# Optimization experiments

Measured on AMD Instinct MI355X. Metric: run time of the kernel, lower is better.

The kernel has to match this reference:

```python
import jax, jax.numpy as jnp
import numpy as np

B, S, V, E, H, L = 32, 512, 32000, 256, 512, 48


def setup_inputs() -> dict:
    key = jax.random.key(0)
    ks = jax.random.split(key, 12)
    tokens = jax.random.randint(ks[0], (B, S), 0, V)
    length = jax.random.randint(ks[1], (B,), S // 2, S + 1)
    labels = jax.random.randint(ks[2], (B, S), 0, L)
    embed_table = jax.random.normal(ks[3], (V, E), jnp.float32) * 0.1
    embed_table = embed_table.at[0].set(0.0)  # padding_idx = 0
    # torch LSTM gate order: i, f, g, o ; b = b_ih + b_hh folded together
    w_ih_f = jax.random.normal(ks[4], (4 * H, E), jnp.float32) * 0.05
    w_hh_f = jax.random.normal(ks[5], (4 * H, H), jnp.float32) * 0.05
    b_f = jnp.zeros((4 * H,), jnp.float32)
    w_ih_b = jax.random.normal(ks[6], (4 * H, E), jnp.float32) * 0.05
    w_hh_b = jax.random.normal(ks[7], (4 * H, H), jnp.float32) * 0.05
    b_b = jnp.zeros((4 * H,), jnp.float32)
    w_em = jax.random.normal(ks[8], (L, 2 * H), jnp.float32) * 0.02
    b_em = jnp.zeros((L,), jnp.float32)
    transition = jax.random.uniform(ks[9], (L, L), jnp.float32)  # torch.rand init
    return {"tokens": tokens, "length": length, "labels": labels,
            "embed_table": embed_table,
            "w_ih_f": w_ih_f, "w_hh_f": w_hh_f, "b_f": b_f,
            "w_ih_b": w_ih_b, "w_hh_b": w_hh_b, "b_b": b_b,
            "w_em": w_em, "b_em": b_em, "transition": transition}


def _lstm_dir(x, w_ih, w_hh, b, reverse):
    # x: [B,S,E] -> hidden states [B,S,H]
    xw = jnp.einsum('bse,ge->bsg', x, w_ih) + b  # precompute input projection [B,S,4H]
    if reverse:
        xw = xw[:, ::-1]
    Bn = x.shape[0]
    Hn = w_hh.shape[1]
    h0 = jnp.zeros((Bn, Hn), x.dtype)
    c0 = jnp.zeros((Bn, Hn), x.dtype)

    def step(carry, xt):
        h, c = carry
        gates = xt + h @ w_hh.T  # [B,4H]
        i, f, g, o = jnp.split(gates, 4, axis=-1)
        i = jax.nn.sigmoid(i)
        f = jax.nn.sigmoid(f)
        g = jnp.tanh(g)
        o = jax.nn.sigmoid(o)
        c = f * c + i * g
        h = o * jnp.tanh(c)
        return (h, c), h

    _, hs = jax.lax.scan(step, (h0, c0), jnp.swapaxes(xw, 0, 1))
    hs = jnp.swapaxes(hs, 0, 1)  # [B,S,H]
    if reverse:
        hs = hs[:, ::-1]
    return hs


def reference(tokens, length, labels, embed_table,
              w_ih_f, w_hh_f, b_f, w_ih_b, w_hh_b, b_b,
              w_em, b_em, transition):
    x = embed_table[tokens]                      # [B,S,E]
    hf = _lstm_dir(x, w_ih_f, w_hh_f, b_f, reverse=False)
    hb = _lstm_dir(x, w_ih_b, w_hh_b, b_b, reverse=True)
    h = jnp.concatenate([hf, hb], axis=-1)       # [B,S,2H]
    logits = jnp.einsum('bsh,lh->bsl', h, w_em) + b_em
    e = jnp.exp(logits)                          # emission = exp(linear), as in source
    T = jnp.exp(transition)                      # transition = exp(param), as in source
    Bn, Sn = tokens.shape
    pos = jnp.arange(Sn)[None, :]
    mask = pos < length[:, None]                 # [B,S] valid positions

    # gold path score: sum emissions over valid steps + transitions between them
    em_real = jnp.take_along_axis(e, labels[..., None], axis=-1)[..., 0]  # [B,S]
    real = jnp.sum(em_real * mask, axis=-1)
    trans_real = T[labels[:, :-1], labels[:, 1:]]                          # [B,S-1]
    real = real + jnp.sum(trans_real * mask[:, 1:], axis=-1)

    # forward algorithm, exactly as written in source:
    # alpha_new[k] = logsumexp_l( alpha[k] + T[k,l] + e_t[l] )
    alpha0 = e[:, 0, :]                          # [B,L]

    def step(alpha, inp):
        et, mt = inp                             # [B,L], [B]
        scores = alpha[:, :, None] + T[None, :, :] + et[:, None, :]  # [B,L,L]
        new = jax.nn.logsumexp(scores, axis=-1)
        alpha = jnp.where(mt[:, None], new, alpha)
        return alpha, None

    alpha, _ = jax.lax.scan(step, alpha0,
                            (jnp.swapaxes(e[:, 1:], 0, 1),
                             jnp.swapaxes(mask[:, 1:], 0, 1)))
    sum_score = jax.nn.logsumexp(alpha, axis=-1)  # [B]
    return sum_score - real                       # negative log probability per example
```

## Files before the change

kernel.cpp:

```cpp
#include <hip/hip_runtime.h>
#include <math.h>
#include <stdint.h>

#define Bn 32
#define Sn 512
#define En 256
#define Hn 512
#define Ln 48
#define G4 2048
#define NWG 32
#define SENT16 0x7FFFu

typedef unsigned short u16;
typedef __attribute__((ext_vector_type(8))) __bf16 bf16x8;
typedef __attribute__((ext_vector_type(4))) float f32x4;

__device__ inline float bf2f(u16 u) {
    return __uint_as_float(((unsigned)u) << 16);
}
__device__ inline u16 f2bf(float f) {
    unsigned u = __float_as_uint(f);
    unsigned r = (u + 0x7fffu + ((u >> 16) & 1u)) >> 16;
    return (u16)r;
}
__device__ inline float sigmoidf_(float x) { return 1.f / (1.f + expf(-x)); }
__device__ inline float tanh_fast(float x) { return 2.f / (1.f + expf(-2.f * x)) - 1.f; }

__device__ inline unsigned badMask(f32x4 v) {
    unsigned acc = 0;
    #pragma unroll
    for (int i = 0; i < 4; i++) {
        unsigned d = __float_as_uint(v[i]);
        unsigned x = d ^ 0x7FFF7FFFu;
        acc |= (x - 0x00010001u) & ~x & 0x80008000u;
    }
    return acc;
}

__global__ __launch_bounds__(256) void prep_kernel(
    const int* __restrict__ tokens, const float* __restrict__ embed,
    const float* __restrict__ wihf, const float* __restrict__ wihb,
    const float* __restrict__ whhf, const float* __restrict__ whhb,
    const float* __restrict__ wem, const float* __restrict__ trans,
    u16* __restrict__ xbf, u16* __restrict__ wihf_b, u16* __restrict__ wihb_b,
    u16* __restrict__ whhf_b, u16* __restrict__ whhb_b, u16* __restrict__ wem_b,
    float* __restrict__ expT, float* __restrict__ alphaAcc,
    float* __restrict__ realAcc, unsigned* __restrict__ hf32,
    unsigned* __restrict__ hb32)
{
    size_t idx = (size_t)blockIdx.x * blockDim.x + threadIdx.x;
    size_t stride = (size_t)gridDim.x * blockDim.x;
    for (size_t i = idx; i < (size_t)Bn * Sn * En; i += stride) {
        size_t n = i >> 8; int ee = (int)(i & 255);
        int tok = tokens[n];
        xbf[i] = f2bf(embed[(size_t)tok * En + ee]);
    }
    for (size_t i = idx; i < (size_t)G4 * En; i += stride) {
        wihf_b[i] = f2bf(wihf[i]); wihb_b[i] = f2bf(wihb[i]);
    }
    for (size_t i = idx; i < (size_t)G4 * Hn; i += stride) {
        whhf_b[i] = f2bf(whhf[i]); whhb_b[i] = f2bf(whhb[i]);
    }
    for (size_t i = idx; i < (size_t)Ln * 2 * Hn; i += stride) wem_b[i] = f2bf(wem[i]);
    for (size_t i = idx; i < (size_t)Ln * Ln; i += stride) expT[i] = expf(trans[i]);
    for (size_t i = idx; i < (size_t)Bn * Ln; i += stride) alphaAcc[i] = 0.f;
    for (size_t i = idx; i < (size_t)Bn; i += stride) realAcc[i] = 0.f;
    const unsigned sp = (SENT16 << 16) | SENT16;
    for (size_t i = idx; i < (size_t)Bn * Sn * Hn / 2; i += stride) {
        hf32[i] = sp; hb32[i] = sp;
    }
}

__global__ __launch_bounds__(256) void gemm_xw(
    const u16* __restrict__ xbf, const u16* __restrict__ wihf_b,
    const u16* __restrict__ wihb_b, const float* __restrict__ bias_f,
    const float* __restrict__ bias_b, u16* __restrict__ xw_f, u16* __restrict__ xw_b)
{
    int mb = blockIdx.x, nb = blockIdx.y, dir = blockIdx.z;
    const u16* wih = dir ? wihb_b : wihf_b;
    const float* bias = dir ? bias_b : bias_f;
    u16* xw = dir ? xw_b : xw_f;

    __shared__ u16 As[128 * 72];
    __shared__ u16 Bs[128 * 72];

    int tid = threadIdx.x;
    int w = tid >> 6, lane = tid & 63;
    int lm = lane & 15, kq = lane >> 4;
    int Moff = (w & 1) * 64, Noff = (w >> 1) * 64;

    f32x4 zero = {0.f, 0.f, 0.f, 0.f};
    f32x4 acc[4][4];
    #pragma unroll
    for (int mi = 0; mi < 4; mi++)
        #pragma unroll
        for (int ni = 0; ni < 4; ni++) acc[mi][ni] = zero;

    for (int kc = 0; kc < 4; kc++) {
        #pragma unroll
        for (int it = 0; it < 4; it++) {
            int idx = tid + it * 256;
            int r = idx >> 3, pos = (idx & 7) * 8;
            *(bf16x8*)&As[r * 72 + pos] =
                *(const bf16x8*)&xbf[((size_t)(mb * 128 + r)) * En + kc * 64 + pos];
            *(bf16x8*)&Bs[r * 72 + pos] =
                *(const bf16x8*)&wih[((size_t)(nb * 128 + r)) * En + kc * 64 + pos];
        }
        __syncthreads();
        #pragma unroll
        for (int ks = 0; ks < 2; ks++) {
            int k = ks * 32 + kq * 8;
            bf16x8 af[4], bfr[4];
            #pragma unroll
            for (int mi = 0; mi < 4; mi++)
                af[mi] = *(const bf16x8*)&As[(Moff + mi * 16 + lm) * 72 + k];
            #pragma unroll
            for (int ni = 0; ni < 4; ni++)
                bfr[ni] = *(const bf16x8*)&Bs[(Noff + ni * 16 + lm) * 72 + k];
            #pragma unroll
            for (int mi = 0; mi < 4; mi++)
                #pragma unroll
                for (int ni = 0; ni < 4; ni++)
                    acc[mi][ni] = __builtin_amdgcn_mfma_f32_16x16x32_bf16(
                        af[mi], bfr[ni], acc[mi][ni], 0, 0, 0);
        }
        __syncthreads();
    }
    #pragma unroll
    for (int mi = 0; mi < 4; mi++)
        #pragma unroll
        for (int ni = 0; ni < 4; ni++)
            #pragma unroll
            for (int reg = 0; reg < 4; reg++) {
                int row = Moff + mi * 16 + kq * 4 + reg;
                int col = Noff + ni * 16 + lm;
                int n = mb * 128 + row;
                int g = nb * 128 + col;
                int t = n & 511, b = n >> 9;
                float v = acc[mi][ni][reg] + bias[g];
                xw[((size_t)t * Bn + b) * G4 + g] = f2bf(v);
            }
}

__global__ __launch_bounds__(512) void lstm_rec(
    const u16* __restrict__ whhf_b, const u16* __restrict__ whhb_b,
    const u16* __restrict__ xw_f, const u16* __restrict__ xw_b,
    u16* __restrict__ hf, u16* __restrict__ hb)
{
    int wg = blockIdx.x;
    int dir = wg >> 5;
    int w = wg & 31;
    const u16* __restrict__ whh = dir ? whhb_b : whhf_b;
    const u16* __restrict__ xw  = dir ? xw_b  : xw_f;
    u16* __restrict__ hbuf = dir ? hb : hf;

    __shared__ u16 Hs[32 * 512];
    __shared__ float Cp[4 * 32 * 17];
    __shared__ u16 hout[32 * 16];

    int tid = threadIdx.x;
    int wv = tid >> 6, lane = tid & 63;
    int lm = lane & 15, kq = lane >> 4;
    int mt = wv & 1, nt = wv >> 1;
    int b = tid >> 4, hc = tid & 15;

    bf16x8 Bf[16];
    {
        const u16* wrow = &whh[((size_t)nt * Hn + (size_t)w * 16 + lm) * Hn];
        #pragma unroll
        for (int ks = 0; ks < 16; ks++)
            Bf[ks] = *(const bf16x8*)&wrow[ks * 32 + kq * 8];
    }

    float c_state = 0.f;
    const f32x4 zero = {0.f, 0.f, 0.f, 0.f};

    for (int it = 0; it < Sn; it++) {
        int t = dir ? (Sn - 1 - it) : it;
        f32x4 acc = zero;

        const u16* xp = &xw[((size_t)t * Bn + b) * G4 + (size_t)w * 16 + hc];
        float xg0 = bf2f(xp[0 * Hn]);
        float xg1 = bf2f(xp[1 * Hn]);
        float xg2 = bf2f(xp[2 * Hn]);
        float xg3 = bf2f(xp[3 * Hn]);

        if (it > 0) {
            int tprev = dir ? (t + 1) : (t - 1);
            const u16* base = &hbuf[((size_t)b * Sn + tprev) * Hn];
            const u16* p0 = base + (hc + 0) * 8;
            const u16* p1 = base + (hc + 16) * 8;
            const u16* p2 = base + (hc + 32) * 8;
            const u16* p3 = base + (hc + 48) * 8;
            f32x4 h0, h1, h2, h3;
            int tries = 0;
            while (true) {
                asm volatile(
                    "global_load_dwordx4 %0, %4, off sc1\n\t"
                    "global_load_dwordx4 %1, %5, off sc1\n\t"
                    "global_load_dwordx4 %2, %6, off sc1\n\t"
                    "global_load_dwordx4 %3, %7, off sc1\n\t"
                    "s_waitcnt vmcnt(0)"
                    : "=v"(h0), "=v"(h1), "=v"(h2), "=v"(h3)
                    : "v"(p0), "v"(p1), "v"(p2), "v"(p3)
                    : "memory");
                if (!(badMask(h0) | badMask(h1) | badMask(h2) | badMask(h3))) break;
                if (++tries > (1 << 16)) break;
            }
            *(f32x4*)&Hs[(b * 64 + ((hc + 0) ^ (b & 7))) * 8] = h0;
            *(f32x4*)&Hs[(b * 64 + ((hc + 16) ^ (b & 7))) * 8] = h1;
            *(f32x4*)&Hs[(b * 64 + ((hc + 32) ^ (b & 7))) * 8] = h2;
            *(f32x4*)&Hs[(b * 64 + ((hc + 48) ^ (b & 7))) * 8] = h3;
            __syncthreads();

            f32x4 aa = zero, ab = zero;
            #pragma unroll
            for (int ks2 = 0; ks2 < 8; ks2++) {
                bf16x8 a0 = *(const bf16x8*)
                    &Hs[((mt * 16 + lm) * 64 + (((2 * ks2) * 4 + kq) ^ (lm & 7))) * 8];
                aa = __builtin_amdgcn_mfma_f32_16x16x32_bf16(a0, Bf[2 * ks2], aa, 0, 0, 0);
                bf16x8 a1 = *(const bf16x8*)
                    &Hs[((mt * 16 + lm) * 64 + (((2 * ks2 + 1) * 4 + kq) ^ (lm & 7))) * 8];
                ab = __builtin_amdgcn_mfma_f32_16x16x32_bf16(a1, Bf[2 * ks2 + 1], ab, 0, 0, 0);
            }
            acc = aa + ab;
        }

        #pragma unroll
        for (int reg = 0; reg < 4; reg++)
            Cp[(nt * 32 + mt * 16 + kq * 4 + reg) * 17 + lm] = acc[reg];
        __syncthreads();

        float g0 = Cp[(0 * 32 + b) * 17 + hc] + xg0;
        float g1 = Cp[(1 * 32 + b) * 17 + hc] + xg1;
        float g2 = Cp[(2 * 32 + b) * 17 + hc] + xg2;
        float g3 = Cp[(3 * 32 + b) * 17 + hc] + xg3;
        float i_ = sigmoidf_(g0);
        float f_ = sigmoidf_(g1);
        float gg = tanh_fast(g2);
        float o_ = sigmoidf_(g3);
        c_state = f_ * c_state + i_ * gg;
        float hv = o_ * tanh_fast(c_state);
        hout[tid] = f2bf(hv);
        __syncthreads();

        if (tid < 64) {
            int bq = lane >> 1, half = lane & 1;
            f32x4 hv8 = *(const f32x4*)&hout[lane * 8];
            u16* sp = &hbuf[((size_t)bq * Sn + t) * Hn + (size_t)w * 16 + half * 8];
            asm volatile("global_store_dwordx4 %0, %1, off sc1"
                         :: "v"(sp), "v"(hv8) : "memory");
        }
    }
}

__global__ __launch_bounds__(256) void emis_crf(
    const u16* __restrict__ hf, const u16* __restrict__ hb,
    const u16* __restrict__ wem_b, const float* __restrict__ bem,
    const float* __restrict__ expT, const int* __restrict__ labels,
    const int* __restrict__ lengths, float* __restrict__ e0,
    float* __restrict__ alphaAcc, float* __restrict__ realAcc)
{
    int mb = blockIdx.x;
    int b = mb >> 3, t0 = (mb & 7) * 64;

    __shared__ float eL[64][49];
    __shared__ float Ts[48 * 48];
    __shared__ float sred[4][48];
    __shared__ float rred[64];

    int tid = threadIdx.x;
    for (int i = tid; i < 48 * 48; i += 256) Ts[i] = expT[i];

    int wv = tid >> 6, lane = tid & 63;
    int lm = lane & 15, lkq = (lane >> 4) * 8;
    int row = mb * 64 + wv * 16;

    f32x4 zero = {0.f, 0.f, 0.f, 0.f};
    f32x4 acc[3] = {zero, zero, zero};
    for (int ks = 0; ks < 32; ks++) {
        int k = ks * 32 + lkq;
        const u16* hsrc = (ks < 16) ? &hf[(size_t)(row + lm) * Hn + k]
                                    : &hb[(size_t)(row + lm) * Hn + (k - 512)];
        bf16x8 a = *(const bf16x8*)hsrc;
        #pragma unroll
        for (int nt = 0; nt < 3; nt++) {
            bf16x8 bfr = *(const bf16x8*)&wem_b[(size_t)(nt * 16 + lm) * 1024 + k];
            acc[nt] = __builtin_amdgcn_mfma_f32_16x16x32_bf16(a, bfr, acc[nt], 0, 0, 0);
        }
    }
    #pragma unroll
    for (int nt = 0; nt < 3; nt++)
        #pragma unroll
        for (int reg = 0; reg < 4; reg++) {
            int rib = wv * 16 + (lane >> 4) * 4 + reg;
            int col = nt * 16 + lm;
            float v = expf(acc[nt][reg] + bem[col]);
            eL[rib][col] = v;
            if ((mb & 7) == 0 && rib == 0) e0[b * Ln + col] = v;
        }
    __syncthreads();

    int len = lengths[b];
    if (tid < 192) {
        int i = tid % 48, tg = tid / 48;
        float sacc = 0.f;
        for (int p = tg * 16; p < tg * 16 + 16; p++) {
            int t = t0 + p;
            if (t >= 1 && t < len) {
                float m = -1e30f;
                for (int j = 0; j < 48; j++) m = fmaxf(m, Ts[i * 48 + j] + eL[p][j]);
                float s = 0.f;
                for (int j = 0; j < 48; j++) s += expf(Ts[i * 48 + j] + eL[p][j] - m);
                sacc += m + logf(s);
            }
        }
        sred[tg][i] = sacc;
    } else {
        int p = tid - 192;
        int t = t0 + p;
        float r = 0.f;
        if (t < len) {
            int lab = labels[b * Sn + t];
            r = eL[p][lab];
            if (t >= 1) r += Ts[labels[b * Sn + t - 1] * 48 + lab];
        }
        rred[p] = r;
    }
    __syncthreads();
    if (tid < 48) {
        float s = sred[0][tid] + sred[1][tid] + sred[2][tid] + sred[3][tid];
        atomicAdd(&alphaAcc[b * Ln + tid], s);
    } else if (tid == 48) {
        float r = 0.f;
        for (int p = 0; p < 64; p++) r += rred[p];
        atomicAdd(&realAcc[b], r);
    }
}

__global__ __launch_bounds__(64) void finalize(
    const float* __restrict__ e0, const float* __restrict__ alphaAcc,
    const float* __restrict__ realAcc, float* __restrict__ out)
{
    int b = threadIdx.x;
    if (b >= Bn) return;
    float m = -1e30f;
    for (int i = 0; i < Ln; i++) {
        float a = e0[b * Ln + i] + alphaAcc[b * Ln + i];
        m = fmaxf(m, a);
    }
    float s = 0.f;
    for (int i = 0; i < Ln; i++) {
        float a = e0[b * Ln + i] + alphaAcc[b * Ln + i];
        s += expf(a - m);
    }
    out[b] = m + logf(s) - realAcc[b];
}

extern "C" void kernel_launch(void* const* d_in, const int* in_sizes, int n_in,
                              void* d_out, int out_size, void* d_ws, size_t ws_size,
                              hipStream_t stream)
{
    const int*   tokens = (const int*)d_in[0];
    const int*   length = (const int*)d_in[1];
    const int*   labels = (const int*)d_in[2];
    const float* embed  = (const float*)d_in[3];
    const float* wihf   = (const float*)d_in[4];
    const float* whhf   = (const float*)d_in[5];
    const float* bf     = (const float*)d_in[6];
    const float* wihb   = (const float*)d_in[7];
    const float* whhb   = (const float*)d_in[8];
    const float* bbv    = (const float*)d_in[9];
    const float* wem    = (const float*)d_in[10];
    const float* bem    = (const float*)d_in[11];
    const float* trans  = (const float*)d_in[12];
    float* out = (float*)d_out;

    char* p = (char*)d_ws;
    auto take = [&](size_t bytes) -> char* {
        char* q = p;
        p += (bytes + 255) & ~(size_t)255;
        return q;
    };
    u16* xw_f   = (u16*)take((size_t)Sn * Bn * G4 * 2);
    u16* xw_b   = (u16*)take((size_t)Sn * Bn * G4 * 2);
    u16* hf     = (u16*)take((size_t)Bn * Sn * Hn * 2);
    u16* hb     = (u16*)take((size_t)Bn * Sn * Hn * 2);
    u16* xbf    = (u16*)take((size_t)Bn * Sn * En * 2);
    u16* wihf_b = (u16*)take((size_t)G4 * En * 2);
    u16* wihb_b = (u16*)take((size_t)G4 * En * 2);
    u16* whhf_b = (u16*)take((size_t)G4 * Hn * 2);
    u16* whhb_b = (u16*)take((size_t)G4 * Hn * 2);
    u16* wem_b  = (u16*)take((size_t)Ln * 2 * Hn * 2);
    float* expT     = (float*)take((size_t)Ln * Ln * 4);
    float* e0       = (float*)take((size_t)Bn * Ln * 4);
    float* alphaAcc = (float*)take((size_t)Bn * Ln * 4);
    float* realAcc  = (float*)take((size_t)Bn * 4);
    if ((size_t)(p - (char*)d_ws) > ws_size) return;

    prep_kernel<<<4096, 256, 0, stream>>>(tokens, embed, wihf, wihb, whhf, whhb, wem, trans,
                                          xbf, wihf_b, wihb_b, whhf_b, whhb_b, wem_b,
                                          expT, alphaAcc, realAcc,
                                          (unsigned*)hf, (unsigned*)hb);

    dim3 g1(128, 16, 2);
    gemm_xw<<<g1, 256, 0, stream>>>(xbf, wihf_b, wihb_b, bf, bbv, xw_f, xw_b);

    void* ra[] = { (void*)&whhf_b, (void*)&whhb_b, (void*)&xw_f, (void*)&xw_b,
                   (void*)&hf, (void*)&hb };
    hipLaunchCooperativeKernel((const void*)lstm_rec, dim3(2 * NWG), dim3(512), ra, 0, stream);

    emis_crf<<<256, 256, 0, stream>>>(hf, hb, wem_b, bem, expT, labels, length,
                                      e0, alphaAcc, realAcc);
    finalize<<<1, 64, 0, stream>>>(e0, alphaAcc, realAcc, out);
}
```

Before: 1.810 ms.

## Interleave forward and backward LSTM directions in each workgroup with async LDS prefetch

Each of 32 workgroups now runs both the forward and the backward recurrence, alternating half-steps, instead of 64 workgroups each running one direction. While one direction computes, the hidden-state row the other direction needs is prefetched straight into LDS with global_load_lds. Afterwards it is checked for the sentinel and reloaded only if it is stale. The aim is to hide the cross-workgroup global-memory latency on the serial critical path. In exchange, each workgroup does twice the serial work, holds twice the weight registers, and gives up half the parallelism.

```diff
diff --git a/kernel.cpp b/kernel.cpp
--- a/kernel.cpp
+++ b/kernel.cpp
@@ -35,6 +35,57 @@
         acc |= (x - 0x00010001u) & ~x & 0x80008000u;
     }
     return acc;
+}
+
+__device__ inline void wg_barrier() {
+    asm volatile("s_waitcnt lgkmcnt(0)" ::: "memory");
+    __builtin_amdgcn_s_barrier();
+    asm volatile("" ::: "memory");
+}
+__device__ inline void wg_barrier_vm() {
+    asm volatile("s_waitcnt vmcnt(0) lgkmcnt(0)" ::: "memory");
+    __builtin_amdgcn_s_barrier();
+    asm volatile("" ::: "memory");
+}
+
+__device__ inline void gl_lds16(const u16* gsrc, u16* ldst) {
+    __builtin_amdgcn_global_load_lds(
+        (const __attribute__((address_space(1))) unsigned int*)gsrc,
+        (__attribute__((address_space(3))) unsigned int*)ldst,
+        16, 0, 17);
+}
+
+__device__ inline void check_fix(u16* Hsbuf, const u16* rowbase, int b, int hc) {
+    int sw = b & 7;
+    u16* s0 = &Hsbuf[(b * 64 + (hc + 0)) * 8];
+    u16* s1 = &Hsbuf[(b * 64 + (hc + 16)) * 8];
+    u16* s2 = &Hsbuf[(b * 64 + (hc + 32)) * 8];
+    u16* s3 = &Hsbuf[(b * 64 + (hc + 48)) * 8];
+    f32x4 h0 = *(const f32x4*)s0;
+    f32x4 h1 = *(const f32x4*)s1;
+    f32x4 h2 = *(const f32x4*)s2;
+    f32x4 h3 = *(const f32x4*)s3;
+    if (badMask(h0) | badMask(h1) | badMask(h2) | badMask(h3)) {
+        const u16* p0 = rowbase + (size_t)((hc + 0) ^ sw) * 8;
+        const u16* p1 = rowbase + (size_t)((hc + 16) ^ sw) * 8;
+        const u16* p2 = rowbase + (size_t)((hc + 32) ^ sw) * 8;
+        const u16* p3 = rowbase + (size_t)((hc + 48) ^ sw) * 8;
+        int tries = 0;
+        for (;;) {
+            asm volatile(
+                "global_load_dwordx4 %0, %4, off sc1\n\t"
+                "global_load_dwordx4 %1, %5, off sc1\n\t"
+                "global_load_dwordx4 %2, %6, off sc1\n\t"
+                "global_load_dwordx4 %3, %7, off sc1\n\t"
+                "s_waitcnt vmcnt(0)"
+                : "=&v"(h0), "=&v"(h1), "=&v"(h2), "=&v"(h3)
+                : "v"(p0), "v"(p1), "v"(p2), "v"(p3)
+                : "memory");
+            if (!(badMask(h0) | badMask(h1) | badMask(h2) | badMask(h3))) break;
+            if (++tries > (1 << 16)) break;
+        }
+        *(f32x4*)s0 = h0; *(f32x4*)s1 = h1; *(f32x4*)s2 = h2; *(f32x4*)s3 = h3;
+    }
 }
 
 __global__ __launch_bounds__(256) void prep_kernel(
@@ -147,14 +198,10 @@
     const u16* __restrict__ xw_f, const u16* __restrict__ xw_b,
     u16* __restrict__ hf, u16* __restrict__ hb)
 {
-    int wg = blockIdx.x;
-    int dir = wg >> 5;
-    int w = wg & 31;
-    const u16* __restrict__ whh = dir ? whhb_b : whhf_b;
-    const u16* __restrict__ xw  = dir ? xw_b  : xw_f;
-    u16* __restrict__ hbuf = dir ? hb : hf;
-
-    __shared__ u16 Hs[32 * 512];
+    int w = blockIdx.x;
+
+    __shared__ u16 HsF[32 * 512];
+    __shared__ u16 HsB[32 * 512];
     __shared__ float Cp[4 * 32 * 17];
     __shared__ u16 hout[32 * 16];
 
@@ -164,90 +211,125 @@
     int mt = wv & 1, nt = wv >> 1;
     int b = tid >> 4, hc = tid & 15;
 
-    bf16x8 Bf[16];
+    bf16x8 BfF[16], BfB[16];
     {
-        const u16* wrow = &whh[((size_t)nt * Hn + (size_t)w * 16 + lm) * Hn];
-        #pragma unroll
-        for (int ks = 0; ks < 16; ks++)
-            Bf[ks] = *(const bf16x8*)&wrow[ks * 32 + kq * 8];
-    }
-
-    float c_state = 0.f;
+        const u16* wrF = &whhf_b[((size_t)nt * Hn + (size_t)w * 16 + lm) * Hn];
+        const u16* wrB = &whhb_b[((size_t)nt * Hn + (size_t)w * 16 + lm) * Hn];
+        #pragma unroll
+        for (int ks = 0; ks < 16; ks++) {
+            BfF[ks] = *(const bf16x8*)&wrF[ks * 32 + kq * 8];
+            BfB[ks] = *(const bf16x8*)&wrB[ks * 32 + kq * 8];
+        }
+    }
+
+    float cF = 0.f, cB = 0.f;
     const f32x4 zero = {0.f, 0.f, 0.f, 0.f};
 
     for (int it = 0; it < Sn; it++) {
-        int t = dir ? (Sn - 1 - it) : it;
+        int tf = it, tb = Sn - 1 - it;
+
+        wg_barrier_vm();
+        if (it > 0)
+            check_fix(HsF, &hf[((size_t)b * Sn + (tf - 1)) * Hn], b, hc);
+        const u16* xpf = &xw_f[((size_t)tf * Bn + b) * G4 + (size_t)w * 16 + hc];
+        u16 xg0 = xpf[0 * Hn], xg1 = xpf[1 * Hn], xg2 = xpf[2 * Hn], xg3 = xpf[3 * Hn];
+        if (it > 0) {
+            #pragma unroll
+            for (int c = 0; c < 4; c++) {
+                int bb = wv * 4 + c;
+                const u16* rowb = &hb[((size_t)bb * Sn + (tb + 1)) * Hn];
+                gl_lds16(rowb + (size_t)(lane ^ (bb & 7)) * 8, &HsB[bb * 512]);
+            }
+        }
+        wg_barrier();
         f32x4 acc = zero;
-
-        const u16* xp = &xw[((size_t)t * Bn + b) * G4 + (size_t)w * 16 + hc];
-        float xg0 = bf2f(xp[0 * Hn]);
-        float xg1 = bf2f(xp[1 * Hn]);
-        float xg2 = bf2f(xp[2 * Hn]);
-        float xg3 = bf2f(xp[3 * Hn]);
-
         if (it > 0) {
-            int tprev = dir ? (t + 1) : (t - 1);
-            const u16* base = &hbuf[((size_t)b * Sn + tprev) * Hn];
-            const u16* p0 = base + (hc + 0) * 8;
-            const u16* p1 = base + (hc + 16) * 8;
-            const u16* p2 = base + (hc + 32) * 8;
-            const u16* p3 = base + (hc + 48) * 8;
-            f32x4 h0, h1, h2, h3;
-            int tries = 0;
-            while (true) {
-                asm volatile(
-                    "global_load_dwordx4 %0, %4, off sc1\n\t"
-                    "global_load_dwordx4 %1, %5, off sc1\n\t"
-                    "global_load_dwordx4 %2, %6, off sc1\n\t"
-                    "global_load_dwordx4 %3, %7, off sc1\n\t"
-                    "s_waitcnt vmcnt(0)"
-                    : "=v"(h0), "=v"(h1), "=v"(h2), "=v"(h3)
-                    : "v"(p0), "v"(p1), "v"(p2), "v"(p3)
-                    : "memory");
-                if (!(badMask(h0) | badMask(h1) | badMask(h2) | badMask(h3))) break;
-                if (++tries > (1 << 16)) break;
-            }
-            *(f32x4*)&Hs[(b * 64 + ((hc + 0) ^ (b & 7))) * 8] = h0;
-            *(f32x4*)&Hs[(b * 64 + ((hc + 16) ^ (b & 7))) * 8] = h1;
-            *(f32x4*)&Hs[(b * 64 + ((hc + 32) ^ (b & 7))) * 8] = h2;
-            *(f32x4*)&Hs[(b * 64 + ((hc + 48) ^ (b & 7))) * 8] = h3;
-            __syncthreads();
-
             f32x4 aa = zero, ab = zero;
             #pragma unroll
             for (int ks2 = 0; ks2 < 8; ks2++) {
                 bf16x8 a0 = *(const bf16x8*)
-                    &Hs[((mt * 16 + lm) * 64 + (((2 * ks2) * 4 + kq) ^ (lm & 7))) * 8];
-                aa = __builtin_amdgcn_mfma_f32_16x16x32_bf16(a0, Bf[2 * ks2], aa, 0, 0, 0);
+                    &HsF[((mt * 16 + lm) * 64 + (((2 * ks2) * 4 + kq) ^ (lm & 7))) * 8];
+                aa = __builtin_amdgcn_mfma_f32_16x16x32_bf16(a0, BfF[2 * ks2], aa, 0, 0, 0);
                 bf16x8 a1 = *(const bf16x8*)
-                    &Hs[((mt * 16 + lm) * 64 + (((2 * ks2 + 1) * 4 + kq) ^ (lm & 7))) * 8];
-                ab = __builtin_amdgcn_mfma_f32_16x16x32_bf16(a1, Bf[2 * ks2 + 1], ab, 0, 0, 0);
+                    &HsF[((mt * 16 + lm) * 64 + (((2 * ks2 + 1) * 4 + kq) ^ (lm & 7))) * 8];
+                ab = __builtin_amdgcn_mfma_f32_16x16x32_bf16(a1, BfF[2 * ks2 + 1], ab, 0, 0, 0);
             }
             acc = aa + ab;
         }
-
         #pragma unroll
         for (int reg = 0; reg < 4; reg++)
             Cp[(nt * 32 + mt * 16 + kq * 4 + reg) * 17 + lm] = acc[reg];
-        __syncthreads();
-
-        float g0 = Cp[(0 * 32 + b) * 17 + hc] + xg0;
-        float g1 = Cp[(1 * 32 + b) * 17 + hc] + xg1;
-        float g2 = Cp[(2 * 32 + b) * 17 + hc] + xg2;
-        float g3 = Cp[(3 * 32 + b) * 17 + hc] + xg3;
-        float i_ = sigmoidf_(g0);
-        float f_ = sigmoidf_(g1);
-        float gg = tanh_fast(g2);
-        float o_ = sigmoidf_(g3);
-        c_state = f_ * c_state + i_ * gg;
-        float hv = o_ * tanh_fast(c_state);
-        hout[tid] = f2bf(hv);
-        __syncthreads();
-
+        wg_barrier();
+        {
+            float g0 = Cp[(0 * 32 + b) * 17 + hc] + bf2f(xg0);
+            float g1 = Cp[(1 * 32 + b) * 17 + hc] + bf2f(xg1);
+            float g2 = Cp[(2 * 32 + b) * 17 + hc] + bf2f(xg2);
+            float g3 = Cp[(3 * 32 + b) * 17 + hc] + bf2f(xg3);
+            float i_ = sigmoidf_(g0);
+            float f_ = sigmoidf_(g1);
+            float gg = tanh_fast(g2);
+            float o_ = sigmoidf_(g3);
+            cF = f_ * cF + i_ * gg;
+            hout[tid] = f2bf(o_ * tanh_fast(cF));
+        }
+        wg_barrier();
         if (tid < 64) {
             int bq = lane >> 1, half = lane & 1;
             f32x4 hv8 = *(const f32x4*)&hout[lane * 8];
-            u16* sp = &hbuf[((size_t)bq * Sn + t) * Hn + (size_t)w * 16 + half * 8];
+            u16* sp = &hf[((size_t)bq * Sn + tf) * Hn + (size_t)w * 16 + half * 8];
+            asm volatile("global_store_dwordx4 %0, %1, off sc1"
+                         :: "v"(sp), "v"(hv8) : "memory");
+        }
+
+        wg_barrier_vm();
+        if (it > 0)
+            check_fix(HsB, &hb[((size_t)b * Sn + (tb + 1)) * Hn], b, hc);
+        const u16* xpb = &xw_b[((size_t)tb * Bn + b) * G4 + (size_t)w * 16 + hc];
+        u16 yg0 = xpb[0 * Hn], yg1 = xpb[1 * Hn], yg2 = xpb[2 * Hn], yg3 = xpb[3 * Hn];
+        if (it < Sn - 1) {
+            #pragma unroll
+            for (int c = 0; c < 4; c++) {
+                int bb = wv * 4 + c;
+                const u16* rowf = &hf[((size_t)bb * Sn + tf) * Hn];
+                gl_lds16(rowf + (size_t)(lane ^ (bb & 7)) * 8, &HsF[bb * 512]);
+            }
+        }
+        wg_barrier();
+        acc = zero;
+        if (it > 0) {
+            f32x4 aa = zero, ab = zero;
+            #pragma unroll
+            for (int ks2 = 0; ks2 < 8; ks2++) {
+                bf16x8 a0 = *(const bf16x8*)
+                    &HsB[((mt * 16 + lm) * 64 + (((2 * ks2) * 4 + kq) ^ (lm & 7))) * 8];
+                aa = __builtin_amdgcn_mfma_f32_16x16x32_bf16(a0, BfB[2 * ks2], aa, 0, 0, 0);
+                bf16x8 a1 = *(const bf16x8*)
+                    &HsB[((mt * 16 + lm) * 64 + (((2 * ks2 + 1) * 4 + kq) ^ (lm & 7))) * 8];
+                ab = __builtin_amdgcn_mfma_f32_16x16x32_bf16(a1, BfB[2 * ks2 + 1], ab, 0, 0, 0);
+            }
+            acc = aa + ab;
+        }
+        #pragma unroll
+        for (int reg = 0; reg < 4; reg++)
+            Cp[(nt * 32 + mt * 16 + kq * 4 + reg) * 17 + lm] = acc[reg];
+        wg_barrier();
+        {
+            float g0 = Cp[(0 * 32 + b) * 17 + hc] + bf2f(yg0);
+            float g1 = Cp[(1 * 32 + b) * 17 + hc] + bf2f(yg1);
+            float g2 = Cp[(2 * 32 + b) * 17 + hc] + bf2f(yg2);
+            float g3 = Cp[(3 * 32 + b) * 17 + hc] + bf2f(yg3);
+            float i_ = sigmoidf_(g0);
+            float f_ = sigmoidf_(g1);
+            float gg = tanh_fast(g2);
+            float o_ = sigmoidf_(g3);
+            cB = f_ * cB + i_ * gg;
+            hout[tid] = f2bf(o_ * tanh_fast(cB));
+        }
+        wg_barrier();
+        if (tid >= 64 && tid < 128) {
+            int bq = lane >> 1, half = lane & 1;
+            f32x4 hv8 = *(const f32x4*)&hout[lane * 8];
+            u16* sp = &hb[((size_t)bq * Sn + tb) * Hn + (size_t)w * 16 + half * 8];
             asm volatile("global_store_dwordx4 %0, %1, off sc1"
                          :: "v"(sp), "v"(hv8) : "memory");
         }
@@ -408,7 +490,7 @@
 
     void* ra[] = { (void*)&whhf_b, (void*)&whhb_b, (void*)&xw_f, (void*)&xw_b,
                    (void*)&hf, (void*)&hb };
-    hipLaunchCooperativeKernel((const void*)lstm_rec, dim3(2 * NWG), dim3(512), ra, 0, stream);
+    hipLaunchCooperativeKernel((const void*)lstm_rec, dim3(NWG), dim3(512), ra, 0, stream);
 
     emis_crf<<<256, 256, 0, stream>>>(hf, hb, wem_b, bem, expT, labels, length,
                                       e0, alphaAcc, realAcc);
```

Result: slower. 2.767 ms (+52.8%).

## Place each LSTM direction on a single XCD via claim-based team assignment

Applied to the files above, without the earlier changes.

Replaces the cooperative launch with an oversubscribed grid where workgroups read their XCC id, claim slots per XCD, and the first two XCDs to fill 32 slots become the forward and backward teams. Keeping a direction's 32 workgroups on one XCD lets hidden-state exchange go through that XCD's shared L2, so polling first uses sc0 loads and stores are written at both scopes. This removes cross-XCD coherence latency from the per-step recurrence sync. The cost is extra idle workgroups, spin-waits on role assignment, a risk of deadlock if an XCD cannot hold 32 resident workgroups, and dependence on the hardware dispatch pattern.

```diff
diff --git a/kernel.cpp b/kernel.cpp
--- a/kernel.cpp
+++ b/kernel.cpp
@@ -8,7 +8,7 @@
 #define Hn 512
 #define Ln 48
 #define G4 2048
-#define NWG 32
+#define CLAIM_G 1024
 #define SENT16 0x7FFFu
 
 typedef unsigned short u16;
@@ -46,7 +46,8 @@
     u16* __restrict__ whhf_b, u16* __restrict__ whhb_b, u16* __restrict__ wem_b,
     float* __restrict__ expT, float* __restrict__ alphaAcc,
     float* __restrict__ realAcc, unsigned* __restrict__ hf32,
-    unsigned* __restrict__ hb32)
+    unsigned* __restrict__ hb32, int* __restrict__ claimCnt,
+    int* __restrict__ teamCnt, int* __restrict__ teamRole)
 {
     size_t idx = (size_t)blockIdx.x * blockDim.x + threadIdx.x;
     size_t stride = (size_t)gridDim.x * blockDim.x;
@@ -65,6 +66,8 @@
     for (size_t i = idx; i < (size_t)Ln * Ln; i += stride) expT[i] = expf(trans[i]);
     for (size_t i = idx; i < (size_t)Bn * Ln; i += stride) alphaAcc[i] = 0.f;
     for (size_t i = idx; i < (size_t)Bn; i += stride) realAcc[i] = 0.f;
+    for (size_t i = idx; i < 16; i += stride) { claimCnt[i] = 0; teamRole[i] = 0; }
+    for (size_t i = idx; i < 1; i += stride) teamCnt[0] = 0;
     const unsigned sp = (SENT16 << 16) | SENT16;
     for (size_t i = idx; i < (size_t)Bn * Sn * Hn / 2; i += stride) {
         hf32[i] = sp; hb32[i] = sp;
@@ -145,11 +148,48 @@
 __global__ __launch_bounds__(512) void lstm_rec(
     const u16* __restrict__ whhf_b, const u16* __restrict__ whhb_b,
     const u16* __restrict__ xw_f, const u16* __restrict__ xw_b,
-    u16* __restrict__ hf, u16* __restrict__ hb)
-{
-    int wg = blockIdx.x;
-    int dir = wg >> 5;
-    int w = wg & 31;
+    u16* __restrict__ hf, u16* __restrict__ hb,
+    int* __restrict__ claimCnt, int* __restrict__ teamCnt,
+    int* __restrict__ teamRole)
+{
+    __shared__ int roleS[2];
+    int tid = threadIdx.x;
+
+    if (tid == 0) {
+        unsigned xcdr;
+        asm volatile("s_getreg_b32 %0, hwreg(HW_REG_XCC_ID)" : "=s"(xcdr));
+        int myx = (int)(xcdr & 15);
+        int slot = __hip_atomic_fetch_add(&claimCnt[myx], 1,
+                                          __ATOMIC_ACQ_REL, __HIP_MEMORY_SCOPE_AGENT);
+        int dir = -1;
+        if (slot < 32) {
+            if (slot == 31) {
+                int ticket = __hip_atomic_fetch_add(teamCnt, 1,
+                                  __ATOMIC_ACQ_REL, __HIP_MEMORY_SCOPE_AGENT);
+                int role = (ticket == 0) ? 1 : (ticket == 1) ? 2 : -1;
+                __hip_atomic_store(&teamRole[myx], role,
+                                   __ATOMIC_RELEASE, __HIP_MEMORY_SCOPE_AGENT);
+                dir = (role > 0) ? role - 1 : -1;
+            } else {
+                int r = 0, guard = 0;
+                for (;;) {
+                    r = __hip_atomic_load(&teamRole[myx],
+                                          __ATOMIC_ACQUIRE, __HIP_MEMORY_SCOPE_AGENT);
+                    if (r != 0) break;
+                    if (++guard > (1 << 22)) break;
+                    __builtin_amdgcn_s_sleep(2);
+                }
+                dir = (r > 0) ? r - 1 : -1;
+            }
+        }
+        roleS[0] = dir;
+        roleS[1] = slot & 31;
+    }
+    __syncthreads();
+    int dir = roleS[0];
+    int w = roleS[1];
+    if (dir < 0) return;
+
     const u16* __restrict__ whh = dir ? whhb_b : whhf_b;
     const u16* __restrict__ xw  = dir ? xw_b  : xw_f;
     u16* __restrict__ hbuf = dir ? hb : hf;
@@ -158,7 +198,6 @@
     __shared__ float Cp[4 * 32 * 17];
     __shared__ u16 hout[32 * 16];
 
-    int tid = threadIdx.x;
     int wv = tid >> 6, lane = tid & 63;
     int lm = lane & 15, kq = lane >> 4;
     int mt = wv & 1, nt = wv >> 1;
@@ -174,6 +213,7 @@
 
     float c_state = 0.f;
     const f32x4 zero = {0.f, 0.f, 0.f, 0.f};
+    int fastLim = 16;
 
     for (int it = 0; it < Sn; it++) {
         int t = dir ? (Sn - 1 - it) : it;
@@ -194,19 +234,32 @@
             const u16* p3 = base + (hc + 48) * 8;
             f32x4 h0, h1, h2, h3;
             int tries = 0;
-            while (true) {
-                asm volatile(
-                    "global_load_dwordx4 %0, %4, off sc1\n\t"
-                    "global_load_dwordx4 %1, %5, off sc1\n\t"
-                    "global_load_dwordx4 %2, %6, off sc1\n\t"
-                    "global_load_dwordx4 %3, %7, off sc1\n\t"
-                    "s_waitcnt vmcnt(0)"
-                    : "=v"(h0), "=v"(h1), "=v"(h2), "=v"(h3)
-                    : "v"(p0), "v"(p1), "v"(p2), "v"(p3)
-                    : "memory");
+            for (;;) {
+                if (tries < fastLim) {
+                    asm volatile(
+                        "global_load_dwordx4 %0, %4, off sc0\n\t"
+                        "global_load_dwordx4 %1, %5, off sc0\n\t"
+                        "global_load_dwordx4 %2, %6, off sc0\n\t"
+                        "global_load_dwordx4 %3, %7, off sc0\n\t"
+                        "s_waitcnt vmcnt(0)"
+                        : "=&v"(h0), "=&v"(h1), "=&v"(h2), "=&v"(h3)
+                        : "v"(p0), "v"(p1), "v"(p2), "v"(p3)
+                        : "memory");
+                } else {
+                    asm volatile(
+                        "global_load_dwordx4 %0, %4, off sc1\n\t"
+                        "global_load_dwordx4 %1, %5, off sc1\n\t"
+                        "global_load_dwordx4 %2, %6, off sc1\n\t"
+                        "global_load_dwordx4 %3, %7, off sc1\n\t"
+                        "s_waitcnt vmcnt(0)"
+                        : "=&v"(h0), "=&v"(h1), "=&v"(h2), "=&v"(h3)
+                        : "v"(p0), "v"(p1), "v"(p2), "v"(p3)
+                        : "memory");
+                }
                 if (!(badMask(h0) | badMask(h1) | badMask(h2) | badMask(h3))) break;
                 if (++tries > (1 << 16)) break;
             }
+            if (it == 1 && tries >= fastLim) fastLim = 0;
             *(f32x4*)&Hs[(b * 64 + ((hc + 0) ^ (b & 7))) * 8] = h0;
             *(f32x4*)&Hs[(b * 64 + ((hc + 16) ^ (b & 7))) * 8] = h1;
             *(f32x4*)&Hs[(b * 64 + ((hc + 32) ^ (b & 7))) * 8] = h2;
@@ -248,8 +301,10 @@
             int bq = lane >> 1, half = lane & 1;
             f32x4 hv8 = *(const f32x4*)&hout[lane * 8];
             u16* sp = &hbuf[((size_t)bq * Sn + t) * Hn + (size_t)w * 16 + half * 8];
-            asm volatile("global_store_dwordx4 %0, %1, off sc1"
-                         :: "v"(sp), "v"(hv8) : "memory");
+            asm volatile(
+                "global_store_dwordx4 %0, %1, off sc0\n\t"
+                "global_store_dwordx4 %0, %1, off sc1"
+                :: "v"(sp), "v"(hv8) : "memory");
         }
     }
 }
@@ -396,19 +451,22 @@
     float* e0       = (float*)take((size_t)Bn * Ln * 4);
     float* alphaAcc = (float*)take((size_t)Bn * Ln * 4);
     float* realAcc  = (float*)take((size_t)Bn * 4);
+    int* claimCnt   = (int*)take(16 * 4);
+    int* teamCnt    = (int*)take(4);
+    int* teamRole   = (int*)take(16 * 4);
     if ((size_t)(p - (char*)d_ws) > ws_size) return;
 
     prep_kernel<<<4096, 256, 0, stream>>>(tokens, embed, wihf, wihb, whhf, whhb, wem, trans,
                                           xbf, wihf_b, wihb_b, whhf_b, whhb_b, wem_b,
                                           expT, alphaAcc, realAcc,
-                                          (unsigned*)hf, (unsigned*)hb);
+                                          (unsigned*)hf, (unsigned*)hb,
+                                          claimCnt, teamCnt, teamRole);
 
     dim3 g1(128, 16, 2);
     gemm_xw<<<g1, 256, 0, stream>>>(xbf, wihf_b, wihb_b, bf, bbv, xw_f, xw_b);
 
-    void* ra[] = { (void*)&whhf_b, (void*)&whhb_b, (void*)&xw_f, (void*)&xw_b,
-                   (void*)&hf, (void*)&hb };
-    hipLaunchCooperativeKernel((const void*)lstm_rec, dim3(2 * NWG), dim3(512), ra, 0, stream);
+    lstm_rec<<<CLAIM_G, 512, 0, stream>>>(whhf_b, whhb_b, xw_f, xw_b, hf, hb,
+                                          claimCnt, teamCnt, teamRole);
 
     emis_crf<<<256, 256, 0, stream>>>(hf, hb, wem_b, bem, expT, labels, length,
                                       e0, alphaAcc, realAcc);
```

Result: slower. 5.739 ms (+217.0%).
